# Performance work log

Hardware: AMD Instinct MI355X
Metric: run time of the kernel (lower is better)

Reference implementation:

```python
import jax, jax.numpy as jnp
import numpy as np

NUM_CODE = 1024
CODE_DIM = 256
COMMITMENT_COST = 0.25
EPS = 1e-12


def _l2norm(v, axis=-1):
    n = jnp.sqrt(jnp.sum(v * v, axis=axis, keepdims=True))
    return v / jnp.maximum(n, EPS)


def setup_inputs() -> dict:
    key = jax.random.key(0)
    k1, k2 = jax.random.split(key)
    x = jax.random.normal(k1, (64, 8, 128, CODE_DIM), dtype=jnp.float32)
    # codebook init: uniform(-1/num_code, 1/num_code) as in torch
    cw = (jax.random.uniform(k2, (NUM_CODE, CODE_DIM), dtype=jnp.float32) * 2.0 - 1.0) / NUM_CODE
    return {"x": x, "codebook_weight": cw}


def reference(x, codebook_weight):
    # x: [B, C, T, D]
    xn = _l2norm(x)                              # normalized encoder output
    cb = _l2norm(codebook_weight)                # [N, D] normalized codebook
    # cosine similarity and nearest-code lookup
    sim = jnp.einsum('bctd,nd->bctn', xn, cb)    # [B, C, T, N]
    code_indices = jnp.argmax(sim, axis=-1)      # [B, C, T] int
    # one-hot @ codebook == direct gather of normalized codebook rows
    quantized = cb[code_indices]                 # [B, C, T, D]
    # VQ losses (both inputs already normalized, matching torch detach semantics in fwd value)
    e_latent = jnp.mean((quantized - xn) ** 2)
    q_latent = jnp.mean((quantized - xn) ** 2)
    loss = q_latent + COMMITMENT_COST * e_latent
    # straight-through estimator (forward value == quantized)
    quantized_st = xn + jax.lax.stop_gradient(quantized - xn)
    # perplexity from code usage histogram (mean of one-hot over B,C,T)
    total = code_indices.size
    counts = jnp.zeros((NUM_CODE,), jnp.float32).at[code_indices.reshape(-1)].add(1.0)
    avg_probs = counts / total
    perplexity = jnp.exp(-jnp.sum(avg_probs * jnp.log(avg_probs + 1e-10)))
    return (loss, quantized_st, perplexity, codebook_weight, code_indices)
```

## Files before the change

### kernel.cpp

```cpp
#include <hip/hip_runtime.h>
#include <math.h>

#define D 256
#define NCODE 1024
#define V_TOTAL 65536
#define EPSF 1e-12f
#define ROWS 32
#define LSTR 260



__global__ __launch_bounds__(256) void normalize_cb(const float* __restrict__ w,
                                                    float* __restrict__ cb_n,
                                                    float* __restrict__ cb_t) {
    const int wave = threadIdx.x >> 6;
    const int lane = threadIdx.x & 63;
    const int row  = blockIdx.x * 4 + wave;
    float4 wv = *(const float4*)(w + (size_t)row * D + lane * 4);
    float s = wv.x * wv.x + wv.y * wv.y + wv.z * wv.z + wv.w * wv.w;
    #pragma unroll
    for (int off = 32; off; off >>= 1) s += __shfl_xor(s, off);
    const float scale = 1.0f / fmaxf(sqrtf(s), EPSF);
    float4 o;
    o.x = wv.x * scale; o.y = wv.y * scale; o.z = wv.z * scale; o.w = wv.w * scale;
    *(float4*)(cb_n + (size_t)row * D + lane * 4) = o;
    const int k = lane * 4;
    cb_t[(size_t)(k + 0) * NCODE + row] = o.x;
    cb_t[(size_t)(k + 1) * NCODE + row] = o.y;
    cb_t[(size_t)(k + 2) * NCODE + row] = o.z;
    cb_t[(size_t)(k + 3) * NCODE + row] = o.w;
}

__global__ __launch_bounds__(256, 4) void vq_main(const float* __restrict__ x,
                                                  const float* __restrict__ cb_t,
                                                  int* __restrict__ idx_ws,
                                                  unsigned int* __restrict__ counts,
                                                  float* __restrict__ loss_acc,
                                                  float* __restrict__ out_idx_f) {
    __shared__ float xl[ROWS * LSTR];
    __shared__ float nrm_s[ROWS];
    const int tid = threadIdx.x;
    const int v0  = blockIdx.x * ROWS;

    const float4* xg = (const float4*)(x + (size_t)v0 * D);
    #pragma unroll
    for (int i = 0; i < 8; ++i) {
        const int f  = tid + i * 256;
        const int m  = f >> 6;
        const int kk = (f & 63) << 2;
        float4 val = xg[f];
        *(float4*)&xl[m * LSTR + kk] = val;
    }
    __syncthreads();

    {
        const int row = tid >> 3, part = tid & 7;
        float ss = 0.f;
        #pragma unroll
        for (int q = 0; q < 8; ++q) {
            float4 xv = *(const float4*)&xl[row * LSTR + part * 32 + q * 4];
            ss += xv.x * xv.x + xv.y * xv.y + xv.z * xv.z + xv.w * xv.w;
        }
        ss += __shfl_xor(ss, 1);
        ss += __shfl_xor(ss, 2);
        ss += __shfl_xor(ss, 4);
        if (part == 0) nrm_s[row] = fmaxf(sqrtf(ss), EPSF);
    }
    __syncthreads();

    const int tn = tid & 31, tm = tid >> 5;
    float best[4]; int bidx[4];
    #pragma unroll
    for (int i = 0; i < 4; ++i) { best[i] = -3.4e38f; bidx[i] = 0; }

    const float* bp = cb_t + tn * 8;

    #pragma unroll 1
    for (int c = 0; c < 4; ++c) {
        const int n0 = c * 256 + tn * 8;
        const float* bc = bp + c * 256;
        float acc[4][8];
        #pragma unroll
        for (int i = 0; i < 4; ++i)
            #pragma unroll
            for (int j = 0; j < 8; ++j) acc[i][j] = 0.f;

        #pragma unroll 2
        for (int k4 = 0; k4 < 64; ++k4) {
            float4 xa[4];
            #pragma unroll
            for (int i = 0; i < 4; ++i)
                xa[i] = *(const float4*)&xl[(tm * 4 + i) * LSTR + k4 * 4];
            #pragma unroll
            for (int kk = 0; kk < 4; ++kk) {
                const float* bk = bc + (size_t)(k4 * 4 + kk) * NCODE;
                float4 b0 = *(const float4*)bk;
                float4 b1 = *(const float4*)(bk + 4);
                #pragma unroll
                for (int i = 0; i < 4; ++i) {
                    const float xv = ((const float*)&xa[i])[kk];
                    acc[i][0] = fmaf(xv, b0.x, acc[i][0]);
                    acc[i][1] = fmaf(xv, b0.y, acc[i][1]);
                    acc[i][2] = fmaf(xv, b0.z, acc[i][2]);
                    acc[i][3] = fmaf(xv, b0.w, acc[i][3]);
                    acc[i][4] = fmaf(xv, b1.x, acc[i][4]);
                    acc[i][5] = fmaf(xv, b1.y, acc[i][5]);
                    acc[i][6] = fmaf(xv, b1.z, acc[i][6]);
                    acc[i][7] = fmaf(xv, b1.w, acc[i][7]);
                }
            }
        }
        #pragma unroll
        for (int i = 0; i < 4; ++i)
            #pragma unroll
            for (int j = 0; j < 8; ++j) {
                if (acc[i][j] > best[i]) { best[i] = acc[i][j]; bidx[i] = n0 + j; }
            }
    }

    #pragma unroll
    for (int off = 16; off; off >>= 1) {
        #pragma unroll
        for (int i = 0; i < 4; ++i) {
            float ov = __shfl_xor(best[i], off);
            int   oi = __shfl_xor(bidx[i], off);
            if (ov > best[i] || (ov == best[i] && oi < bidx[i])) { best[i] = ov; bidx[i] = oi; }
        }
    }

    float lpart = 0.f;
    if (tn == 0) {
        #pragma unroll
        for (int i = 0; i < 4; ++i) {
            const int row = tm * 4 + i;
            const int v   = v0 + row;
            const float sim = best[i] / nrm_s[row];
            lpart += 2.f - 2.f * sim;
            idx_ws[v] = bidx[i];
            out_idx_f[v] = (float)bidx[i];
            atomicAdd(&counts[bidx[i]], 1u);
        }
    }
    #pragma unroll
    for (int off = 32; off; off >>= 1) lpart += __shfl_xor(lpart, off);
    if ((tid & 63) == 0) atomicAdd(loss_acc, lpart);
}

__global__ __launch_bounds__(256) void gather_q(const int* __restrict__ idx_ws,
                                                const float* __restrict__ cb_n,
                                                float* __restrict__ outq) {
    const int wave = threadIdx.x >> 6;
    const int lane = threadIdx.x & 63;
    const int v = blockIdx.x * 4 + wave;
    const int idx = idx_ws[v];
    float4 val = *(const float4*)(cb_n + (size_t)idx * D + lane * 4);
    *(float4*)(outq + (size_t)v * D + lane * 4) = val;
}

__global__ __launch_bounds__(1024) void finalize(const unsigned int* __restrict__ counts,
                                                 const float* __restrict__ loss_acc,
                                                 float* __restrict__ out_loss,
                                                 float* __restrict__ out_perp) {
    __shared__ float red[16];
    const int t = threadIdx.x;
    const float p = (float)counts[t] / 65536.0f;
    float term = p * logf(p + 1e-10f);
    #pragma unroll
    for (int off = 32; off; off >>= 1) term += __shfl_xor(term, off);
    if ((t & 63) == 0) red[t >> 6] = term;
    __syncthreads();
    if (t < 16) {
        float s = red[t];
        #pragma unroll
        for (int off = 8; off; off >>= 1) s += __shfl_xor(s, off);
        if (t == 0) {
            *out_perp = expf(-s);
            *out_loss = 1.25f * (*loss_acc) / 16777216.0f;
        }
    }
}

extern "C" void kernel_launch(void* const* d_in, const int* in_sizes, int n_in,
                              void* d_out, int out_size, void* d_ws, size_t ws_size,
                              hipStream_t stream) {
    const float* x  = (const float*)d_in[0];
    const float* cw = (const float*)d_in[1];
    float* out = (float*)d_out;
    float* ws  = (float*)d_ws;

    float* cb_n          = ws;
    float* cb_t          = ws + 262144;
    int* idx_ws          = (int*)(ws + 524288);
    unsigned int* counts = (unsigned int*)(ws + 589824);
    float* loss_acc      = ws + 590848;

    hipMemsetAsync(counts, 0, (1024 + 1) * sizeof(float), stream);

    normalize_cb<<<256, 256, 0, stream>>>(cw, cb_n, cb_t);
    vq_main<<<2048, 256, 0, stream>>>(x, cb_t, idx_ws, counts, loss_acc,
                                      out + 17039362);
    gather_q<<<16384, 256, 0, stream>>>(idx_ws, cb_n, out + 1);
    finalize<<<1, 1024, 0, stream>>>(counts, loss_acc, out, out + 16777217);
    hipMemcpyAsync(out + 16777218, cw, (size_t)NCODE * D * sizeof(float),
                   hipMemcpyDeviceToDevice, stream);
}
```

Baseline: 648.7 us.

## Stage codebook slabs into LDS via async global-to-LDS double buffering

The similarity GEMM now streams the transposed codebook through a double-buffered LDS slab using global_load_lds, prefetching the next 8-row slab while computing on the current one. The goal is to replace per-thread global/L2 loads of codebook data with shared LDS reads and to overlap fetches with FMAs. In exchange it adds a block-wide barrier per slab (128 per block), raises LDS use, and lowers the occupancy target from 4 to 3 blocks.

```diff
diff --git a/kernel.cpp b/kernel.cpp
--- a/kernel.cpp
+++ b/kernel.cpp
@@ -3,10 +3,16 @@
 
 #define D 256
 #define NCODE 1024
-#define V_TOTAL 65536
 #define EPSF 1e-12f
 #define ROWS 32
 #define LSTR 260
+#define SLABK 8
+#define NSLAB 128
+
+#define GLOAD_LDS16(gp, lp) \
+  __builtin_amdgcn_global_load_lds( \
+      (const __attribute__((address_space(1))) unsigned int*)(const void*)(gp), \
+      (__attribute__((address_space(3))) unsigned int*)(void*)(lp), 16, 0, 0)
 
 
 
@@ -31,16 +37,19 @@
     cb_t[(size_t)(k + 3) * NCODE + row] = o.w;
 }
 
-__global__ __launch_bounds__(256, 4) void vq_main(const float* __restrict__ x,
+__global__ __launch_bounds__(256, 3) void vq_main(const float* __restrict__ x,
                                                   const float* __restrict__ cb_t,
                                                   int* __restrict__ idx_ws,
                                                   unsigned int* __restrict__ counts,
                                                   float* __restrict__ loss_acc,
                                                   float* __restrict__ out_idx_f) {
     __shared__ float xl[ROWS * LSTR];
+    __shared__ float bl[2][SLABK * 256];
     __shared__ float nrm_s[ROWS];
-    const int tid = threadIdx.x;
-    const int v0  = blockIdx.x * ROWS;
+    const int tid  = threadIdx.x;
+    const int wave = tid >> 6;
+    const int lane = tid & 63;
+    const int v0   = blockIdx.x * ROWS;
 
     const float4* xg = (const float4*)(x + (size_t)v0 * D);
     #pragma unroll
@@ -54,6 +63,12 @@
     __syncthreads();
 
     {
+        const float* g = cb_t + (size_t)(wave * 2) * NCODE + lane * 4;
+        GLOAD_LDS16(g,         &bl[0][(wave * 2 + 0) * 256]);
+        GLOAD_LDS16(g + NCODE, &bl[0][(wave * 2 + 1) * 256]);
+    }
+
+    {
         const int row = tid >> 3, part = tid & 7;
         float ss = 0.f;
         #pragma unroll
@@ -73,49 +88,72 @@
     #pragma unroll
     for (int i = 0; i < 4; ++i) { best[i] = -3.4e38f; bidx[i] = 0; }
 
-    const float* bp = cb_t + tn * 8;
+    float acc[4][8];
+    #pragma unroll
+    for (int i = 0; i < 4; ++i)
+        #pragma unroll
+        for (int j = 0; j < 8; ++j) acc[i][j] = 0.f;
+
+    const float* xrow0 = &xl[(tm * 4 + 0) * LSTR];
+    const float* xrow1 = &xl[(tm * 4 + 1) * LSTR];
+    const float* xrow2 = &xl[(tm * 4 + 2) * LSTR];
+    const float* xrow3 = &xl[(tm * 4 + 3) * LSTR];
 
     #pragma unroll 1
-    for (int c = 0; c < 4; ++c) {
-        const int n0 = c * 256 + tn * 8;
-        const float* bc = bp + c * 256;
-        float acc[4][8];
-        #pragma unroll
-        for (int i = 0; i < 4; ++i)
+    for (int s = 0; s < NSLAB; ++s) {
+        if (s) __syncthreads();
+
+        if (s + 1 < NSLAB) {
+            const int c1  = (s + 1) >> 5;
+            const int k01 = ((s + 1) & 31) * SLABK;
+            float* dst = bl[(s + 1) & 1];
+            const float* g = cb_t + (size_t)(k01 + wave * 2) * NCODE + c1 * 256 + lane * 4;
+            GLOAD_LDS16(g,         dst + (wave * 2 + 0) * 256);
+            GLOAD_LDS16(g + NCODE, dst + (wave * 2 + 1) * 256);
+        }
+
+        const float* btn = &bl[s & 1][tn * 8];
+        const int kx0 = (s & 31) * SLABK;
+        #pragma unroll
+        for (int k4 = 0; k4 < 2; ++k4) {
+            float4 xa0 = *(const float4*)(xrow0 + kx0 + k4 * 4);
+            float4 xa1 = *(const float4*)(xrow1 + kx0 + k4 * 4);
+            float4 xa2 = *(const float4*)(xrow2 + kx0 + k4 * 4);
+            float4 xa3 = *(const float4*)(xrow3 + kx0 + k4 * 4);
             #pragma unroll
-            for (int j = 0; j < 8; ++j) acc[i][j] = 0.f;
-
-        #pragma unroll 2
-        for (int k4 = 0; k4 < 64; ++k4) {
-            float4 xa[4];
+            for (int kk = 0; kk < 4; ++kk) {
+                const float* bk = btn + (k4 * 4 + kk) * 256;
+                float4 b0 = *(const float4*)bk;
+                float4 b1 = *(const float4*)(bk + 4);
+                const float xv0 = ((const float*)&xa0)[kk];
+                const float xv1 = ((const float*)&xa1)[kk];
+                const float xv2 = ((const float*)&xa2)[kk];
+                const float xv3 = ((const float*)&xa3)[kk];
+                float xv[4] = {xv0, xv1, xv2, xv3};
+                #pragma unroll
+                for (int i = 0; i < 4; ++i) {
+                    acc[i][0] = fmaf(xv[i], b0.x, acc[i][0]);
+                    acc[i][1] = fmaf(xv[i], b0.y, acc[i][1]);
+                    acc[i][2] = fmaf(xv[i], b0.z, acc[i][2]);
+                    acc[i][3] = fmaf(xv[i], b0.w, acc[i][3]);
+                    acc[i][4] = fmaf(xv[i], b1.x, acc[i][4]);
+                    acc[i][5] = fmaf(xv[i], b1.y, acc[i][5]);
+                    acc[i][6] = fmaf(xv[i], b1.z, acc[i][6]);
+                    acc[i][7] = fmaf(xv[i], b1.w, acc[i][7]);
+                }
+            }
+        }
+
+        if ((s & 31) == 31) {
+            const int n0 = (s >> 5) * 256 + tn * 8;
             #pragma unroll
             for (int i = 0; i < 4; ++i)
-                xa[i] = *(const float4*)&xl[(tm * 4 + i) * LSTR + k4 * 4];
-            #pragma unroll
-            for (int kk = 0; kk < 4; ++kk) {
-                const float* bk = bc + (size_t)(k4 * 4 + kk) * NCODE;
-                float4 b0 = *(const float4*)bk;
-                float4 b1 = *(const float4*)(bk + 4);
                 #pragma unroll
-                for (int i = 0; i < 4; ++i) {
-                    const float xv = ((const float*)&xa[i])[kk];
-                    acc[i][0] = fmaf(xv, b0.x, acc[i][0]);
-                    acc[i][1] = fmaf(xv, b0.y, acc[i][1]);
-                    acc[i][2] = fmaf(xv, b0.z, acc[i][2]);
-                    acc[i][3] = fmaf(xv, b0.w, acc[i][3]);
-                    acc[i][4] = fmaf(xv, b1.x, acc[i][4]);
-                    acc[i][5] = fmaf(xv, b1.y, acc[i][5]);
-                    acc[i][6] = fmaf(xv, b1.z, acc[i][6]);
-                    acc[i][7] = fmaf(xv, b1.w, acc[i][7]);
+                for (int j = 0; j < 8; ++j) {
+                    if (acc[i][j] > best[i]) { best[i] = acc[i][j]; bidx[i] = n0 + j; }
+                    acc[i][j] = 0.f;
                 }
-            }
-        }
-        #pragma unroll
-        for (int i = 0; i < 4; ++i)
-            #pragma unroll
-            for (int j = 0; j < 8; ++j) {
-                if (acc[i][j] > best[i]) { best[i] = acc[i][j]; bidx[i] = n0 + j; }
-            }
+        }
     }
 
     #pragma unroll
```

Result: faster. 587.7 us (-9.4%).
